# Performance work log

Hardware: AMD Instinct MI355X
Metric: run time of the kernel (lower is better)

Reference implementation:

```python
import jax, jax.numpy as jnp
import numpy as np

V, E, C, H = 50000, 300, 128, 128
B, SC, SE = 128, 512, 64


def gru_scan(x, lengths, gate_w, gate_b, cand_w, cand_b):
    """TF GRUCell dynamic_rnn: x [B,S,E] -> outputs [B,S,C], zeroed past lengths."""
    Bn, S, _ = x.shape
    Cn = cand_w.shape[1]

    def step(h, inp):
        xt, t = inp  # xt [B,E]
        ru = jax.nn.sigmoid(jnp.concatenate([xt, h], axis=-1) @ gate_w + gate_b)
        r, u = jnp.split(ru, 2, axis=-1)
        c = jnp.tanh(jnp.concatenate([xt, r * h], axis=-1) @ cand_w + cand_b)
        hn = u * h + (1.0 - u) * c
        active = (t < lengths)[:, None]
        hn = jnp.where(active, hn, h)
        out = jnp.where(active, hn, 0.0)
        return hn, out

    h0 = jnp.zeros((Bn, Cn), dtype=x.dtype)
    _, outs = jax.lax.scan(step, h0, (jnp.swapaxes(x, 0, 1), jnp.arange(S)))
    return jnp.swapaxes(outs, 0, 1)


def reverse_seq(x, lengths):
    """tf.reverse_sequence along time for [B,S,D]."""
    S = x.shape[1]
    t = jnp.arange(S)[None, :]
    L = lengths[:, None]
    idx = jnp.where(t < L, L - 1 - t, t)
    return jnp.take_along_axis(x, idx[:, :, None], axis=1)


def attend(states, att_v, att_w, att_b):
    # states [B,S,C]
    scores = jnp.einsum('bsd,d->bs', jnp.tanh(jnp.einsum('bsc,cd->bsd', states, att_w) + att_b), att_v)
    w = jax.nn.softmax(scores, axis=1)
    return jnp.einsum('bsc,bs->bc', states, w)


def extract_features(seq, lengths, embeddings,
                     fw_gate_w, fw_gate_b, fw_cand_w, fw_cand_b,
                     bw_gate_w, bw_gate_b, bw_cand_w, bw_cand_b,
                     att_v, att_w, att_b):
    emb = embeddings[seq]  # [B,S,E]
    fw_states = gru_scan(emb, lengths, fw_gate_w, fw_gate_b, fw_cand_w, fw_cand_b)
    emb_rev = reverse_seq(emb, lengths)
    bw_out = gru_scan(emb_rev, lengths, bw_gate_w, bw_gate_b, bw_cand_w, bw_cand_b)
    bw_states = reverse_seq(bw_out, lengths)
    fw_c = attend(fw_states, att_v, att_w, att_b)
    bw_c = attend(bw_states, att_v, att_w, att_b)
    return jnp.concatenate([fw_c, bw_c], axis=1)


def setup_inputs() -> dict:
    key = jax.random.key(0)
    ks = jax.random.split(key, 20)
    s = 0.05
    context = jax.random.randint(ks[0], (B, SC), 0, V, dtype=jnp.int32)
    end = jax.random.randint(ks[1], (B, SE), 0, V, dtype=jnp.int32)
    context_length = jnp.clip(jax.random.randint(ks[2], (B,), 1, SC + 1), 1, SC).astype(jnp.int32)
    end_length = jnp.clip(jax.random.randint(ks[3], (B,), 1, SE + 1), 1, SE).astype(jnp.int32)
    return {
        'context': context, 'end': end,
        'context_length': context_length, 'end_length': end_length,
        'embeddings': jax.random.normal(ks[4], (V, E), jnp.float32) * s,
        'fw_gate_w': jax.random.normal(ks[5], (E + C, 2 * C), jnp.float32) * s,
        'fw_gate_b': jnp.ones((2 * C,), jnp.float32),
        'fw_cand_w': jax.random.normal(ks[6], (E + C, C), jnp.float32) * s,
        'fw_cand_b': jnp.zeros((C,), jnp.float32),
        'bw_gate_w': jax.random.normal(ks[7], (E + C, 2 * C), jnp.float32) * s,
        'bw_gate_b': jnp.ones((2 * C,), jnp.float32),
        'bw_cand_w': jax.random.normal(ks[8], (E + C, C), jnp.float32) * s,
        'bw_cand_b': jnp.zeros((C,), jnp.float32),
        'att_v': jax.random.normal(ks[9], (C,), jnp.float32) * s,
        'att_w': jax.random.normal(ks[10], (C, C), jnp.float32) * s,
        'att_b': jnp.zeros((C,), jnp.float32),
        'hid_w': jax.random.normal(ks[11], (4 * C, H), jnp.float32) * s,
        'hid_b': jnp.zeros((H,), jnp.float32),
        'out_w': jax.random.normal(ks[12], (H, 1), jnp.float32) * s,
        'out_b': jnp.zeros((1,), jnp.float32),
    }


def reference(context, end, context_length, end_length, embeddings,
              fw_gate_w, fw_gate_b, fw_cand_w, fw_cand_b,
              bw_gate_w, bw_gate_b, bw_cand_w, bw_cand_b,
              att_v, att_w, att_b, hid_w, hid_b, out_w, out_b):
    ctx_f = extract_features(context, context_length, embeddings,
                             fw_gate_w, fw_gate_b, fw_cand_w, fw_cand_b,
                             bw_gate_w, bw_gate_b, bw_cand_w, bw_cand_b,
                             att_v, att_w, att_b)
    end_f = extract_features(end, end_length, embeddings,
                             fw_gate_w, fw_gate_b, fw_cand_w, fw_cand_b,
                             bw_gate_w, bw_gate_b, bw_cand_w, bw_cand_b,
                             att_v, att_w, att_b)
    feats = jnp.concatenate([ctx_f, end_f], axis=1)  # [B, 4C]
    hidden = jax.nn.relu(feats @ hid_w + hid_b)
    logit = (hidden @ out_w + out_b)[:, 0]  # [B]
    return logit
```

## Files before the change

### kernel.cpp

```cpp
#include <hip/hip_runtime.h>
#include <cstdint>
#include <cmath>

static constexpr int V_  = 50000;
static constexpr int E_  = 300;
static constexpr int C_  = 128;
static constexpr int B_  = 128;
static constexpr int SC_ = 512;
static constexpr int SE_ = 64;
static constexpr int NCOL = 768;
static constexpr int KP  = 320;

static constexpr size_t OFF_PROJ  = 0;
static constexpr size_t SZ_PROJ   = (size_t)V_ * NCOL;
static constexpr size_t OFF_WXP   = OFF_PROJ + SZ_PROJ;
static constexpr size_t SZ_WXP    = (size_t)304 * NCOL;
static constexpr size_t OFF_UALL  = OFF_WXP + SZ_WXP;
static constexpr size_t SZ_UALL   = (size_t)C_ * NCOL;
static constexpr size_t OFF_BIAS  = OFF_UALL + SZ_UALL;
static constexpr size_t SZ_BIAS   = NCOL;
static constexpr size_t OFF_ST    = OFF_BIAS + SZ_BIAS;
static constexpr size_t SZ_ST_CTX = (size_t)B_ * SC_ * C_;
static constexpr size_t SZ_ST_END = (size_t)B_ * SE_ * C_;
static constexpr size_t SZ_ST     = 2*SZ_ST_CTX + 2*SZ_ST_END;
static constexpr size_t OFF_FEATS = OFF_ST + SZ_ST;
static constexpr size_t SZ_FEATS  = (size_t)B_ * 512;
static constexpr size_t OFF_BT    = OFF_FEATS + SZ_FEATS;
static constexpr size_t SZ_BT     = (size_t)NCOL * KP / 2 * 2;
static constexpr size_t OFF_AWT   = OFF_BT + SZ_BT;

typedef __attribute__((ext_vector_type(8))) short bf16x8;
typedef __attribute__((ext_vector_type(4))) float f32x4;

static __device__ __forceinline__ unsigned short f2bf_rne(float f) {
  unsigned u = __float_as_uint(f);
  unsigned r = u + 0x7fffu + ((u >> 16) & 1u);
  return (unsigned short)(r >> 16);
}

static __device__ __forceinline__ void gload_lds16(const short* g, short* l) {
  __builtin_amdgcn_global_load_lds(
      (const __attribute__((address_space(1))) void*)g,
      (__attribute__((address_space(3))) void*)l, 16, 0, 0);
}

static __device__ __forceinline__ float fast_sigmoid(float x) {
  return __builtin_amdgcn_rcpf(1.f + __expf(-x));
}
static __device__ __forceinline__ float fast_tanh(float x) {
  return fmaf(-2.f, __builtin_amdgcn_rcpf(__expf(2.f * x) + 1.f), 1.f);
}

__global__ void pack_kernel(const float* __restrict__ fw_gw, const float* __restrict__ fw_gb,
                            const float* __restrict__ fw_cw, const float* __restrict__ fw_cb,
                            const float* __restrict__ bw_gw, const float* __restrict__ bw_gb,
                            const float* __restrict__ bw_cw, const float* __restrict__ bw_cb,
                            float* __restrict__ ws) {
  int i = blockIdx.x * 256 + threadIdx.x;
  float* Wxp  = ws + OFF_WXP;
  float* Uall = ws + OFF_UALL;
  float* bias = ws + OFF_BIAS;
  if (i < 304 * NCOL) {
    int k = i / NCOL, c = i % NCOL;
    float v = 0.f;
    if (k < 300) {
      if (c < 256)      v = fw_gw[k*256 + c];
      else if (c < 384) v = fw_cw[k*128 + (c-256)];
      else if (c < 640) v = bw_gw[k*256 + (c-384)];
      else              v = bw_cw[k*128 + (c-640)];
    }
    Wxp[i] = v;
    return;
  }
  int j = i - 304 * NCOL;
  if (j >= 0 && j < 128 * NCOL) {
    int k = j / NCOL, c = j % NCOL;
    int kk = 300 + k;
    float v;
    if (c < 256)      v = fw_gw[kk*256 + c];
    else if (c < 384) v = fw_cw[kk*128 + (c-256)];
    else if (c < 640) v = bw_gw[kk*256 + (c-384)];
    else              v = bw_cw[kk*128 + (c-640)];
    Uall[j] = v;
    return;
  }
  int m = j - 128 * NCOL;
  if (m >= 0 && m < NCOL) {
    float v;
    if (m < 256)      v = fw_gb[m];
    else if (m < 384) v = fw_cb[m-256];
    else if (m < 640) v = bw_gb[m-384];
    else              v = bw_cb[m-640];
    bias[m] = v;
  }
}

__global__ void pack_bt(const float* __restrict__ Wxp, short* __restrict__ Bthi,
                        short* __restrict__ Btlo, const float* __restrict__ att_w,
                        short* __restrict__ awt_hi, short* __restrict__ awt_lo) {
  int i = blockIdx.x * 256 + threadIdx.x;
  if (i < NCOL * KP) {
    int k = i % KP, n = i / KP;
    float v = (k < 304) ? Wxp[(size_t)k * NCOL + n] : 0.f;
    unsigned short h = f2bf_rne(v);
    float hf = __uint_as_float((unsigned)h << 16);
    unsigned short lo = f2bf_rne(v - hf);
    Bthi[i] = (short)h;
    Btlo[i] = (short)lo;
    return;
  }
  int j = i - NCOL * KP;
  if (j < 128 * 128) {
    int d = j >> 7, c = j & 127;
    float v = att_w[(size_t)c * 128 + d];
    unsigned short h = f2bf_rne(v);
    float hf = __uint_as_float((unsigned)h << 16);
    unsigned short lo = f2bf_rne(v - hf);
    awt_hi[j] = (short)h;
    awt_lo[j] = (short)lo;
  }
}

__global__ void pack_emb(const float* __restrict__ emb, short* __restrict__ Ahi,
                         short* __restrict__ Alo) {
  size_t i = (size_t)blockIdx.x * 256 + threadIdx.x;
  if (i >= (size_t)V_ * KP) return;
  int k = (int)(i % KP);
  size_t row = i / KP;
  float v = (k < E_) ? emb[row * E_ + k] : 0.f;
  unsigned short h = f2bf_rne(v);
  float hf = __uint_as_float((unsigned)h << 16);
  unsigned short lo = f2bf_rne(v - hf);
  Ahi[i] = (short)h;
  Alo[i] = (short)lo;
}

__global__ __launch_bounds__(256) void gemm_mfma(
    const short* __restrict__ Ahi, const short* __restrict__ Alo,
    const short* __restrict__ Bthi, const short* __restrict__ Btlo,
    float* __restrict__ proj) {
  __shared__ short lds[16384];
  int tid = threadIdx.x, wid = tid >> 6, lane = tid & 63;
  int n0 = blockIdx.x * 128, m0 = blockIdx.y * 128;
  f32x4 acc[4][4] = {};

  int lr = lane >> 2, lc = lane & 3;
  int q0 = wid * 2, q1 = q0 + 1;
  int r0 = q0 * 16 + lr, r1 = q1 * 16 + lr;
  int am0 = m0 + r0; if (am0 > V_ - 1) am0 = V_ - 1;
  int am1 = m0 + r1; if (am1 > V_ - 1) am1 = V_ - 1;
  size_t gaOff0 = (size_t)am0 * KP + lc * 8;
  size_t gaOff1 = (size_t)am1 * KP + lc * 8;
  size_t gbOff0 = (size_t)(n0 + r0) * KP + lc * 8;
  size_t gbOff1 = (size_t)(n0 + r1) * KP + lc * 8;

  int quad = lane >> 4;
  int arow = (wid >> 1) * 64 + (lane & 15);
  int brow = (wid & 1) * 64 + (lane & 15);

  for (int k0 = 0; k0 < KP; k0 += 32) {
    gload_lds16(Ahi  + gaOff0 + k0, lds +         q0 * 512);
    gload_lds16(Ahi  + gaOff1 + k0, lds +         q1 * 512);
    gload_lds16(Alo  + gaOff0 + k0, lds +  4096 + q0 * 512);
    gload_lds16(Alo  + gaOff1 + k0, lds +  4096 + q1 * 512);
    gload_lds16(Bthi + gbOff0 + k0, lds +  8192 + q0 * 512);
    gload_lds16(Bthi + gbOff1 + k0, lds +  8192 + q1 * 512);
    gload_lds16(Btlo + gbOff0 + k0, lds + 12288 + q0 * 512);
    gload_lds16(Btlo + gbOff1 + k0, lds + 12288 + q1 * 512);
    __syncthreads();

    bf16x8 ah[4], al[4], bh[4], bl[4];
#pragma unroll
    for (int i = 0; i < 4; ++i) {
      ah[i] = *(bf16x8*)&lds[        (arow + i*16) * 32 + quad * 8];
      al[i] = *(bf16x8*)&lds[ 4096 + (arow + i*16) * 32 + quad * 8];
      bh[i] = *(bf16x8*)&lds[ 8192 + (brow + i*16) * 32 + quad * 8];
      bl[i] = *(bf16x8*)&lds[12288 + (brow + i*16) * 32 + quad * 8];
    }
#pragma unroll
    for (int i = 0; i < 4; ++i)
#pragma unroll
      for (int j = 0; j < 4; ++j) {
        acc[i][j] = __builtin_amdgcn_mfma_f32_16x16x32_bf16(ah[i], bh[j], acc[i][j], 0, 0, 0);
        acc[i][j] = __builtin_amdgcn_mfma_f32_16x16x32_bf16(ah[i], bl[j], acc[i][j], 0, 0, 0);
        acc[i][j] = __builtin_amdgcn_mfma_f32_16x16x32_bf16(al[i], bh[j], acc[i][j], 0, 0, 0);
      }
    __syncthreads();
  }

  int colb = n0 + (wid & 1) * 64 + (lane & 15);
  int rowb = m0 + (wid >> 1) * 64 + quad * 4;
#pragma unroll
  for (int i = 0; i < 4; ++i) {
    int rb = rowb + i * 16;
#pragma unroll
    for (int j = 0; j < 4; ++j) {
      int cc = colb + j * 16;
#pragma unroll
      for (int r = 0; r < 4; ++r) {
        int rr = rb + r;
        if (rr < V_) proj[(size_t)rr * NCOL + cc] = acc[i][j][r];
      }
    }
  }
}

__global__ __attribute__((amdgpu_flat_work_group_size(256, 256),
                          amdgpu_waves_per_eu(2, 2)))
void recur_kernel(
    const int* __restrict__ ctx, const int* __restrict__ endseq,
    const int* __restrict__ ctx_len, const int* __restrict__ end_len,
    const float* __restrict__ proj, const float* __restrict__ Uall,
    const float* __restrict__ bias, float* __restrict__ states) {
  __shared__ __align__(16) float h_s[128];
  __shared__ __align__(16) float rh_s[128];
  __shared__ __align__(16) float u_s[128];
  __shared__ __align__(16) float pg[8][260];
  __shared__ __align__(16) float pc[8][132];

  int bid = blockIdx.x;
  int tid = threadIdx.x;
  const int* seq; int S, L, b, dir; float* stbase;
  if (bid < 256) {
    b = bid >> 1; dir = bid & 1;
    seq = ctx + b * SC_; S = SC_; L = ctx_len[b];
    stbase = states + (dir ? SZ_ST_CTX : 0) + (size_t)b * SC_ * C_;
  } else {
    int q = bid - 256; b = q >> 1; dir = q & 1;
    seq = endseq + b * SE_; S = SE_; L = end_len[b];
    stbase = states + 2*SZ_ST_CTX + (dir ? SZ_ST_END : 0) + (size_t)b * SE_ * C_;
  }
  int dirOff = dir ? 384 : 0;
  int kg = tid >> 5, jg = tid & 31;

  float wg[16][8];
  float wc[16][4];
#pragma unroll
  for (int kk = 0; kk < 16; ++kk) {
    const float* up = Uall + (size_t)(kg*16 + kk) * NCOL + dirOff;
    float4 w0 = *(const float4*)(up + jg*8);
    float4 w1 = *(const float4*)(up + jg*8 + 4);
    wg[kk][0]=w0.x; wg[kk][1]=w0.y; wg[kk][2]=w0.z; wg[kk][3]=w0.w;
    wg[kk][4]=w1.x; wg[kk][5]=w1.y; wg[kk][6]=w1.z; wg[kk][7]=w1.w;
    float4 wv = *(const float4*)(up + 256 + jg*4);
    wc[kk][0]=wv.x; wc[kk][1]=wv.y; wc[kk][2]=wv.z; wc[kk][3]=wv.w;
  }
  float bias_g = bias[dirOff + tid];
  float bias_c = (tid < 128) ? bias[dirOff + 256 + tid] : 0.f;

  if (tid < 128) h_s[tid] = 0.f;
  __syncthreads();

  int pos0 = dir ? (L - 1) : 0;
  int tok0 = seq[pos0];
  const float* xr0 = proj + (size_t)tok0 * NCOL + dirOff;
  float xg = xr0[tid];
  float xc = (tid < 128) ? xr0[256 + tid] : 0.f;

  for (int t = 0; t < L; ++t) {
    float xg_n = 0.f, xc_n = 0.f;
    if (t + 1 < L) {
      int pos_n = dir ? (L - 2 - t) : (t + 1);
      int tok_n = seq[pos_n];
      const float* xr = proj + (size_t)tok_n * NCOL + dirOff;
      xg_n = xr[tid];
      xc_n = (tid < 128) ? xr[256 + tid] : 0.f;
    }

    float a[8] = {0.f,0.f,0.f,0.f,0.f,0.f,0.f,0.f};
    const float4* h4 = (const float4*)h_s;
#pragma unroll
    for (int q = 0; q < 4; ++q) {
      float4 hv = h4[kg*4 + q];
      float he[4] = {hv.x, hv.y, hv.z, hv.w};
#pragma unroll
      for (int e = 0; e < 4; ++e)
#pragma unroll
        for (int jj = 0; jj < 8; ++jj)
          a[jj] += he[e] * wg[q*4 + e][jj];
    }
    *(float4*)(&pg[kg][jg*8])     = make_float4(a[0], a[1], a[2], a[3]);
    *(float4*)(&pg[kg][jg*8 + 4]) = make_float4(a[4], a[5], a[6], a[7]);
    __syncthreads();

    float g = xg + bias_g;
#pragma unroll
    for (int k2 = 0; k2 < 8; ++k2) g += pg[k2][tid];
    g = fast_sigmoid(g);

    float h_old = 0.f;
    if (tid < 128) { h_old = h_s[tid]; rh_s[tid] = g * h_old; }
    else           { u_s[tid - 128] = g; }
    __syncthreads();

    float ac[4] = {0.f, 0.f, 0.f, 0.f};
    const float4* rh4 = (const float4*)rh_s;
#pragma unroll
    for (int q = 0; q < 4; ++q) {
      float4 rv = rh4[kg*4 + q];
      float re[4] = {rv.x, rv.y, rv.z, rv.w};
#pragma unroll
      for (int e = 0; e < 4; ++e)
#pragma unroll
        for (int jj = 0; jj < 4; ++jj)
          ac[jj] += re[e] * wc[q*4 + e][jj];
    }
    *(float4*)(&pc[kg][jg*4]) = make_float4(ac[0], ac[1], ac[2], ac[3]);
    __syncthreads();

    if (tid < 128) {
      float cs = xc + bias_c;
#pragma unroll
      for (int k2 = 0; k2 < 8; ++k2) cs += pc[k2][tid];
      float c = fast_tanh(cs);
      float u = u_s[tid];
      float hn = u * h_old + (1.f - u) * c;
      h_s[tid] = hn;
      int pos = dir ? (L - 1 - t) : t;
      stbase[(size_t)pos * C_ + tid] = hn;
    }
    __syncthreads();
    xg = xg_n; xc = xc_n;
  }

  for (int i = L * C_ + tid; i < S * C_; i += 256) stbase[i] = 0.f;
}

__global__ __launch_bounds__(256, 2) void attn_kernel(
    const float* __restrict__ states, const short* __restrict__ awt_hi,
    const short* __restrict__ awt_lo, const float* __restrict__ att_v,
    const float* __restrict__ att_b, float* __restrict__ feats) {
  __shared__ __align__(16) float st_s[16][132];
  __shared__ __align__(16) short ah_s[16][132];
  __shared__ __align__(16) short al_s[16][132];
  __shared__ float spart[4][16];
  __shared__ float score_s[16];
  __shared__ float cm[128], cl[128], ca[128];

  int bid = blockIdx.x, tid = threadIdx.x;
  int b, dir, S, featOff; const float* stb;
  if (bid < 256) {
    b = bid >> 1; dir = bid & 1; S = SC_;
    stb = states + (dir ? SZ_ST_CTX : 0) + (size_t)b * SC_ * C_;
    featOff = dir * 128;
  } else {
    int q = bid - 256; b = q >> 1; dir = q & 1; S = SE_;
    stb = states + 2*SZ_ST_CTX + (dir ? SZ_ST_END : 0) + (size_t)b * SE_ * C_;
    featOff = 256 + dir * 128;
  }

  int w = tid >> 6, lane = tid & 63;
  int quad = lane >> 4, l15 = lane & 15;

  int d0 = 32 * w + l15, d1 = d0 + 16;
  bf16x8 bh0[4], bh1[4], bl0[4], bl1[4];
#pragma unroll
  for (int kt = 0; kt < 4; ++kt) {
    bh0[kt] = *(const bf16x8*)&awt_hi[d0*128 + kt*32 + quad*8];
    bh1[kt] = *(const bf16x8*)&awt_hi[d1*128 + kt*32 + quad*8];
    bl0[kt] = *(const bf16x8*)&awt_lo[d0*128 + kt*32 + quad*8];
    bl1[kt] = *(const bf16x8*)&awt_lo[d1*128 + kt*32 + quad*8];
  }
  float vv0 = att_v[d0], vv1 = att_v[d1];
  float bb0 = att_b[d0], bb1 = att_b[d1];

  int c = tid & 127, half = tid >> 7;
  float m = -1e30f, lsum = 0.f, acc = 0.f;

  int lrow = tid >> 4, lcol = (tid & 15) * 8;
  float4 p0, p1;
  {
    const float* src = stb + (size_t)lrow * C_ + lcol;
    p0 = *(const float4*)(src);
    p1 = *(const float4*)(src + 4);
  }

  int nchunks = S >> 4;
  for (int ch = 0; ch < nchunks; ++ch) {
    __syncthreads();
    float f[8] = {p0.x, p0.y, p0.z, p0.w, p1.x, p1.y, p1.z, p1.w};
    short hi8[8], lo8[8];
#pragma unroll
    for (int j = 0; j < 8; ++j) {
      unsigned short h = f2bf_rne(f[j]);
      float hf = __uint_as_float((unsigned)h << 16);
      hi8[j] = (short)h;
      lo8[j] = (short)f2bf_rne(f[j] - hf);
    }
    *(float4*)(&st_s[lrow][lcol])     = p0;
    *(float4*)(&st_s[lrow][lcol + 4]) = p1;
    *(bf16x8*)(&ah_s[lrow][lcol]) = *(bf16x8*)hi8;
    *(bf16x8*)(&al_s[lrow][lcol]) = *(bf16x8*)lo8;
    if (ch + 1 < nchunks) {
      const float* src = stb + (size_t)((ch + 1) * 16 + lrow) * C_ + lcol;
      p0 = *(const float4*)(src);
      p1 = *(const float4*)(src + 4);
    }
    __syncthreads();

    f32x4 ac0 = {0.f, 0.f, 0.f, 0.f}, ac1 = {0.f, 0.f, 0.f, 0.f};
#pragma unroll
    for (int kt = 0; kt < 4; ++kt) {
      bf16x8 a_hi = *(bf16x8*)&ah_s[l15][kt*32 + quad*8];
      bf16x8 a_lo = *(bf16x8*)&al_s[l15][kt*32 + quad*8];
      ac0 = __builtin_amdgcn_mfma_f32_16x16x32_bf16(a_hi, bh0[kt], ac0, 0, 0, 0);
      ac0 = __builtin_amdgcn_mfma_f32_16x16x32_bf16(a_hi, bl0[kt], ac0, 0, 0, 0);
      ac0 = __builtin_amdgcn_mfma_f32_16x16x32_bf16(a_lo, bh0[kt], ac0, 0, 0, 0);
      ac1 = __builtin_amdgcn_mfma_f32_16x16x32_bf16(a_hi, bh1[kt], ac1, 0, 0, 0);
      ac1 = __builtin_amdgcn_mfma_f32_16x16x32_bf16(a_hi, bl1[kt], ac1, 0, 0, 0);
      ac1 = __builtin_amdgcn_mfma_f32_16x16x32_bf16(a_lo, bh1[kt], ac1, 0, 0, 0);
    }

    float part[4];
#pragma unroll
    for (int r = 0; r < 4; ++r)
      part[r] = fast_tanh(ac0[r] + bb0) * vv0 + fast_tanh(ac1[r] + bb1) * vv1;
#pragma unroll
    for (int mask = 1; mask <= 8; mask <<= 1)
#pragma unroll
      for (int r = 0; r < 4; ++r)
        part[r] += __shfl_xor(part[r], mask, 64);
    if (l15 == 0) {
#pragma unroll
      for (int r = 0; r < 4; ++r) spart[w][quad*4 + r] = part[r];
    }
    __syncthreads();
    if (tid < 16)
      score_s[tid] = spart[0][tid] + spart[1][tid] + spart[2][tid] + spart[3][tid];
    __syncthreads();

    float srow[8]; float smax = m;
#pragma unroll
    for (int r = 0; r < 8; ++r) { srow[r] = score_s[half*8 + r]; smax = fmaxf(smax, srow[r]); }
    float scale = __expf(m - smax);
    acc *= scale; lsum *= scale; m = smax;
#pragma unroll
    for (int r = 0; r < 8; ++r) {
      float wgt = __expf(srow[r] - m);
      lsum += wgt;
      acc += wgt * st_s[half*8 + r][c];
    }
  }

  __syncthreads();
  if (half == 1) { cm[c] = m; cl[c] = lsum; ca[c] = acc; }
  __syncthreads();
  if (half == 0) {
    float m1 = cm[c], l1 = cl[c], a1 = ca[c];
    float M = fmaxf(m, m1);
    float w0 = __expf(m - M), w1 = __expf(m1 - M);
    feats[b * 512 + featOff + c] = (acc * w0 + a1 * w1) / (lsum * w0 + l1 * w1);
  }
}

__global__ __launch_bounds__(128) void head_kernel(
    const float* __restrict__ feats, const float* __restrict__ hid_w,
    const float* __restrict__ hid_b, const float* __restrict__ out_w,
    const float* __restrict__ out_b, float* __restrict__ out) {
  __shared__ __align__(16) float f_s[512];
  __shared__ float part[2];
  int b = blockIdx.x, tid = threadIdx.x;
  for (int i = tid; i < 512; i += 128) f_s[i] = feats[b * 512 + i];
  __syncthreads();
  float h = hid_b[tid];
  for (int k = 0; k < 512; ++k) h += f_s[k] * hid_w[k * 128 + tid];
  h = fmaxf(h, 0.f);
  float p = h * out_w[tid];
#pragma unroll
  for (int off = 32; off > 0; off >>= 1) p += __shfl_xor(p, off, 64);
  if ((tid & 63) == 0) part[tid >> 6] = p;
  __syncthreads();
  if (tid == 0) out[b] = part[0] + part[1] + out_b[0];
}

extern "C" void kernel_launch(void* const* d_in, const int* in_sizes, int n_in,
                              void* d_out, int out_size, void* d_ws, size_t ws_size,
                              hipStream_t stream) {
  const int*   ctx     = (const int*)d_in[0];
  const int*   endseq  = (const int*)d_in[1];
  const int*   ctx_len = (const int*)d_in[2];
  const int*   end_len = (const int*)d_in[3];
  const float* emb     = (const float*)d_in[4];
  const float* fw_gw   = (const float*)d_in[5];
  const float* fw_gb   = (const float*)d_in[6];
  const float* fw_cw   = (const float*)d_in[7];
  const float* fw_cb   = (const float*)d_in[8];
  const float* bw_gw   = (const float*)d_in[9];
  const float* bw_gb   = (const float*)d_in[10];
  const float* bw_cw   = (const float*)d_in[11];
  const float* bw_cb   = (const float*)d_in[12];
  const float* att_v   = (const float*)d_in[13];
  const float* att_w   = (const float*)d_in[14];
  const float* att_b   = (const float*)d_in[15];
  const float* hid_w   = (const float*)d_in[16];
  const float* hid_b   = (const float*)d_in[17];
  const float* out_w   = (const float*)d_in[18];
  const float* out_b   = (const float*)d_in[19];
  float* ws  = (float*)d_ws;
  float* out = (float*)d_out;

  short* Ahi    = (short*)(ws + OFF_ST);
  short* Alo    = Ahi + (size_t)V_ * KP;
  short* Bthi   = (short*)(ws + OFF_BT);
  short* Btlo   = Bthi + (size_t)NCOL * KP;
  short* awt_hi = (short*)(ws + OFF_AWT);
  short* awt_lo = awt_hi + 128 * 128;

  pack_kernel<<<1299, 256, 0, stream>>>(fw_gw, fw_gb, fw_cw, fw_cb,
                                        bw_gw, bw_gb, bw_cw, bw_cb, ws);
  pack_bt<<<(NCOL * KP + 128 * 128 + 255) / 256, 256, 0, stream>>>(
      ws + OFF_WXP, Bthi, Btlo, att_w, awt_hi, awt_lo);
  pack_emb<<<(int)(((size_t)V_ * KP + 255) / 256), 256, 0, stream>>>(emb, Ahi, Alo);

  dim3 ggrid(6, 391);
  gemm_mfma<<<ggrid, 256, 0, stream>>>(Ahi, Alo, Bthi, Btlo, ws + OFF_PROJ);

  recur_kernel<<<512, 256, 0, stream>>>(ctx, endseq, ctx_len, end_len,
                                        ws + OFF_PROJ, ws + OFF_UALL,
                                        ws + OFF_BIAS, ws + OFF_ST);

  attn_kernel<<<512, 256, 0, stream>>>(ws + OFF_ST, awt_hi, awt_lo,
                                       att_v, att_b, ws + OFF_FEATS);

  head_kernel<<<128, 128, 0, stream>>>(ws + OFF_FEATS, hid_w, hid_b,
                                       out_w, out_b, out);
}
```

Before: 768.4 us.

## Process two batch sequences per recurrence block to share register-held weights

The GRU recurrence kernel now runs two batch rows (same direction) in each workgroup. The recurrent weights held in registers are reused for both sequences' matvecs, and each barrier covers both sequences. This halves the grid to 256 blocks and gives each wave more independent work to hide latency. In exchange the loop runs to the longer of the two lengths, so the shorter sequence does wasted steps, and waves-per-EU drops to one.

```diff
diff --git a/kernel.cpp b/kernel.cpp
--- a/kernel.cpp
+++ b/kernel.cpp
@@ -206,29 +206,37 @@
 }
 
 __global__ __attribute__((amdgpu_flat_work_group_size(256, 256),
-                          amdgpu_waves_per_eu(2, 2)))
-void recur_kernel(
+                          amdgpu_waves_per_eu(1, 1)))
+void recur_pair_kernel(
     const int* __restrict__ ctx, const int* __restrict__ endseq,
     const int* __restrict__ ctx_len, const int* __restrict__ end_len,
     const float* __restrict__ proj, const float* __restrict__ Uall,
     const float* __restrict__ bias, float* __restrict__ states) {
-  __shared__ __align__(16) float h_s[128];
-  __shared__ __align__(16) float rh_s[128];
-  __shared__ __align__(16) float u_s[128];
-  __shared__ __align__(16) float pg[8][260];
-  __shared__ __align__(16) float pc[8][132];
+  __shared__ __align__(16) float h_sA[128],  h_sB[128];
+  __shared__ __align__(16) float rh_sA[128], rh_sB[128];
+  __shared__ __align__(16) float u_sA[128],  u_sB[128];
+  __shared__ __align__(16) float pgA[8][260], pgB[8][260];
+  __shared__ __align__(16) float pcA[8][132], pcB[8][132];
 
   int bid = blockIdx.x;
   int tid = threadIdx.x;
-  const int* seq; int S, L, b, dir; float* stbase;
-  if (bid < 256) {
-    b = bid >> 1; dir = bid & 1;
-    seq = ctx + b * SC_; S = SC_; L = ctx_len[b];
-    stbase = states + (dir ? SZ_ST_CTX : 0) + (size_t)b * SC_ * C_;
+  const int *seqA, *seqB; int S, LA, LB, dir; float *stA, *stB;
+  if (bid < 128) {
+    dir = bid & 1; int p = bid >> 1;
+    int b0 = p * 2, b1 = b0 + 1;
+    seqA = ctx + b0 * SC_; seqB = ctx + b1 * SC_;
+    S = SC_; LA = ctx_len[b0]; LB = ctx_len[b1];
+    float* base = states + (dir ? SZ_ST_CTX : 0);
+    stA = base + (size_t)b0 * SC_ * C_;
+    stB = base + (size_t)b1 * SC_ * C_;
   } else {
-    int q = bid - 256; b = q >> 1; dir = q & 1;
-    seq = endseq + b * SE_; S = SE_; L = end_len[b];
-    stbase = states + 2*SZ_ST_CTX + (dir ? SZ_ST_END : 0) + (size_t)b * SE_ * C_;
+    int q = bid - 128; dir = q & 1; int p = q >> 1;
+    int b0 = p * 2, b1 = b0 + 1;
+    seqA = endseq + b0 * SE_; seqB = endseq + b1 * SE_;
+    S = SE_; LA = end_len[b0]; LB = end_len[b1];
+    float* base = states + 2*SZ_ST_CTX + (dir ? SZ_ST_END : 0);
+    stA = base + (size_t)b0 * SE_ * C_;
+    stB = base + (size_t)b1 * SE_ * C_;
   }
   int dirOff = dir ? 384 : 0;
   int kg = tid >> 5, jg = tid & 31;
@@ -248,82 +256,131 @@
   float bias_g = bias[dirOff + tid];
   float bias_c = (tid < 128) ? bias[dirOff + 256 + tid] : 0.f;
 
-  if (tid < 128) h_s[tid] = 0.f;
+  if (tid < 128) { h_sA[tid] = 0.f; h_sB[tid] = 0.f; }
   __syncthreads();
 
-  int pos0 = dir ? (L - 1) : 0;
-  int tok0 = seq[pos0];
-  const float* xr0 = proj + (size_t)tok0 * NCOL + dirOff;
-  float xg = xr0[tid];
-  float xc = (tid < 128) ? xr0[256 + tid] : 0.f;
-
-  for (int t = 0; t < L; ++t) {
-    float xg_n = 0.f, xc_n = 0.f;
-    if (t + 1 < L) {
-      int pos_n = dir ? (L - 2 - t) : (t + 1);
-      int tok_n = seq[pos_n];
+  int Lm = (LA > LB) ? LA : LB;
+
+  int posA0 = dir ? (LA - 1) : 0;
+  int tokA0 = seqA[posA0];
+  const float* xrA0 = proj + (size_t)tokA0 * NCOL + dirOff;
+  float xgA = xrA0[tid];
+  float xcA = (tid < 128) ? xrA0[256 + tid] : 0.f;
+  int posB0 = dir ? (LB - 1) : 0;
+  int tokB0 = seqB[posB0];
+  const float* xrB0 = proj + (size_t)tokB0 * NCOL + dirOff;
+  float xgB = xrB0[tid];
+  float xcB = (tid < 128) ? xrB0[256 + tid] : 0.f;
+
+  for (int t = 0; t < Lm; ++t) {
+    float xgA_n = 0.f, xcA_n = 0.f, xgB_n = 0.f, xcB_n = 0.f;
+    if (t + 1 < LA) {
+      int pos_n = dir ? (LA - 2 - t) : (t + 1);
+      int tok_n = seqA[pos_n];
       const float* xr = proj + (size_t)tok_n * NCOL + dirOff;
-      xg_n = xr[tid];
-      xc_n = (tid < 128) ? xr[256 + tid] : 0.f;
-    }
-
-    float a[8] = {0.f,0.f,0.f,0.f,0.f,0.f,0.f,0.f};
-    const float4* h4 = (const float4*)h_s;
+      xgA_n = xr[tid];
+      xcA_n = (tid < 128) ? xr[256 + tid] : 0.f;
+    }
+    if (t + 1 < LB) {
+      int pos_n = dir ? (LB - 2 - t) : (t + 1);
+      int tok_n = seqB[pos_n];
+      const float* xr = proj + (size_t)tok_n * NCOL + dirOff;
+      xgB_n = xr[tid];
+      xcB_n = (tid < 128) ? xr[256 + tid] : 0.f;
+    }
+
+    float aA[8] = {0.f,0.f,0.f,0.f,0.f,0.f,0.f,0.f};
+    float aB[8] = {0.f,0.f,0.f,0.f,0.f,0.f,0.f,0.f};
+    const float4* h4A = (const float4*)h_sA;
+    const float4* h4B = (const float4*)h_sB;
 #pragma unroll
     for (int q = 0; q < 4; ++q) {
-      float4 hv = h4[kg*4 + q];
-      float he[4] = {hv.x, hv.y, hv.z, hv.w};
+      float4 hvA = h4A[kg*4 + q];
+      float4 hvB = h4B[kg*4 + q];
+      float heA[4] = {hvA.x, hvA.y, hvA.z, hvA.w};
+      float heB[4] = {hvB.x, hvB.y, hvB.z, hvB.w};
 #pragma unroll
       for (int e = 0; e < 4; ++e)
 #pragma unroll
-        for (int jj = 0; jj < 8; ++jj)
-          a[jj] += he[e] * wg[q*4 + e][jj];
-    }
-    *(float4*)(&pg[kg][jg*8])     = make_float4(a[0], a[1], a[2], a[3]);
-    *(float4*)(&pg[kg][jg*8 + 4]) = make_float4(a[4], a[5], a[6], a[7]);
-    __syncthreads();
-
-    float g = xg + bias_g;
-#pragma unroll
-    for (int k2 = 0; k2 < 8; ++k2) g += pg[k2][tid];
-    g = fast_sigmoid(g);
-
-    float h_old = 0.f;
-    if (tid < 128) { h_old = h_s[tid]; rh_s[tid] = g * h_old; }
-    else           { u_s[tid - 128] = g; }
-    __syncthreads();
-
-    float ac[4] = {0.f, 0.f, 0.f, 0.f};
-    const float4* rh4 = (const float4*)rh_s;
+        for (int jj = 0; jj < 8; ++jj) {
+          aA[jj] += heA[e] * wg[q*4 + e][jj];
+          aB[jj] += heB[e] * wg[q*4 + e][jj];
+        }
+    }
+    *(float4*)(&pgA[kg][jg*8])     = make_float4(aA[0], aA[1], aA[2], aA[3]);
+    *(float4*)(&pgA[kg][jg*8 + 4]) = make_float4(aA[4], aA[5], aA[6], aA[7]);
+    *(float4*)(&pgB[kg][jg*8])     = make_float4(aB[0], aB[1], aB[2], aB[3]);
+    *(float4*)(&pgB[kg][jg*8 + 4]) = make_float4(aB[4], aB[5], aB[6], aB[7]);
+    __syncthreads();
+
+    float gA = xgA + bias_g;
+    float gB = xgB + bias_g;
+#pragma unroll
+    for (int k2 = 0; k2 < 8; ++k2) { gA += pgA[k2][tid]; gB += pgB[k2][tid]; }
+    gA = fast_sigmoid(gA);
+    gB = fast_sigmoid(gB);
+
+    float h_oldA = 0.f, h_oldB = 0.f;
+    if (tid < 128) {
+      h_oldA = h_sA[tid]; rh_sA[tid] = gA * h_oldA;
+      h_oldB = h_sB[tid]; rh_sB[tid] = gB * h_oldB;
+    } else {
+      u_sA[tid - 128] = gA;
+      u_sB[tid - 128] = gB;
+    }
+    __syncthreads();
+
+    float acA[4] = {0.f, 0.f, 0.f, 0.f};
+    float acB[4] = {0.f, 0.f, 0.f, 0.f};
+    const float4* rh4A = (const float4*)rh_sA;
+    const float4* rh4B = (const float4*)rh_sB;
 #pragma unroll
     for (int q = 0; q < 4; ++q) {
-      float4 rv = rh4[kg*4 + q];
-      float re[4] = {rv.x, rv.y, rv.z, rv.w};
+      float4 rvA = rh4A[kg*4 + q];
+      float4 rvB = rh4B[kg*4 + q];
+      float reA[4] = {rvA.x, rvA.y, rvA.z, rvA.w};
+      float reB[4] = {rvB.x, rvB.y, rvB.z, rvB.w};
 #pragma unroll
       for (int e = 0; e < 4; ++e)
 #pragma unroll
-        for (int jj = 0; jj < 4; ++jj)
-          ac[jj] += re[e] * wc[q*4 + e][jj];
-    }
-    *(float4*)(&pc[kg][jg*4]) = make_float4(ac[0], ac[1], ac[2], ac[3]);
+        for (int jj = 0; jj < 4; ++jj) {
+          acA[jj] += reA[e] * wc[q*4 + e][jj];
+          acB[jj] += reB[e] * wc[q*4 + e][jj];
+        }
+    }
+    *(float4*)(&pcA[kg][jg*4]) = make_float4(acA[0], acA[1], acA[2], acA[3]);
+    *(float4*)(&pcB[kg][jg*4]) = make_float4(acB[0], acB[1], acB[2], acB[3]);
     __syncthreads();
 
     if (tid < 128) {
-      float cs = xc + bias_c;
-#pragma unroll
-      for (int k2 = 0; k2 < 8; ++k2) cs += pc[k2][tid];
-      float c = fast_tanh(cs);
-      float u = u_s[tid];
-      float hn = u * h_old + (1.f - u) * c;
-      h_s[tid] = hn;
-      int pos = dir ? (L - 1 - t) : t;
-      stbase[(size_t)pos * C_ + tid] = hn;
-    }
-    __syncthreads();
-    xg = xg_n; xc = xc_n;
-  }
-
-  for (int i = L * C_ + tid; i < S * C_; i += 256) stbase[i] = 0.f;
+      float csA = xcA + bias_c;
+      float csB = xcB + bias_c;
+#pragma unroll
+      for (int k2 = 0; k2 < 8; ++k2) { csA += pcA[k2][tid]; csB += pcB[k2][tid]; }
+      float cA = fast_tanh(csA);
+      float cB = fast_tanh(csB);
+      float uA = u_sA[tid];
+      float uB = u_sB[tid];
+      float hnA = uA * h_oldA + (1.f - uA) * cA;
+      float hnB = uB * h_oldB + (1.f - uB) * cB;
+      h_sA[tid] = hnA;
+      h_sB[tid] = hnB;
+      if (t < LA) {
+        int pos = dir ? (LA - 1 - t) : t;
+        stA[(size_t)pos * C_ + tid] = hnA;
+      }
+      if (t < LB) {
+        int pos = dir ? (LB - 1 - t) : t;
+        stB[(size_t)pos * C_ + tid] = hnB;
+      }
+    }
+    __syncthreads();
+    xgA = xgA_n; xcA = xcA_n;
+    xgB = xgB_n; xcB = xcB_n;
+  }
+
+  for (int i = LA * C_ + tid; i < S * C_; i += 256) stA[i] = 0.f;
+  for (int i = LB * C_ + tid; i < S * C_; i += 256) stB[i] = 0.f;
 }
 
 __global__ __launch_bounds__(256, 2) void attn_kernel(
@@ -515,9 +572,9 @@
   dim3 ggrid(6, 391);
   gemm_mfma<<<ggrid, 256, 0, stream>>>(Ahi, Alo, Bthi, Btlo, ws + OFF_PROJ);
 
-  recur_kernel<<<512, 256, 0, stream>>>(ctx, endseq, ctx_len, end_len,
-                                        ws + OFF_PROJ, ws + OFF_UALL,
-                                        ws + OFF_BIAS, ws + OFF_ST);
+  recur_pair_kernel<<<256, 256, 0, stream>>>(ctx, endseq, ctx_len, end_len,
+                                             ws + OFF_PROJ, ws + OFF_UALL,
+                                             ws + OFF_BIAS, ws + OFF_ST);
 
   attn_kernel<<<512, 256, 0, stream>>>(ws + OFF_ST, awt_hi, awt_lo,
                                        att_v, att_b, ws + OFF_FEATS);
```

New measurement: 1.068 ms. 1.39x slower.

## Repartition GRU recurrence matvec to pairs of lanes with shuffle reduction

Applied to the files above, without the earlier changes.

Replaces the 8-way k-split matvec with LDS partial-sum buffers by a per-thread layout where each thread owns one gate column (and one candidate column shared by a lane pair) over half the hidden dimension. A new pack kernel rearranges the recurrent weights so each thread loads its slice contiguously into registers. Partial sums are combined with a single lane shuffle instead of LDS writes, which removes two of the four barriers per timestep on the serial critical path. It adds a small extra pack launch and redundant candidate work on both lanes of each pair.

```diff
diff --git a/kernel.cpp b/kernel.cpp
--- a/kernel.cpp
+++ b/kernel.cpp
@@ -28,6 +28,8 @@
 static constexpr size_t OFF_BT    = OFF_FEATS + SZ_FEATS;
 static constexpr size_t SZ_BT     = (size_t)NCOL * KP / 2 * 2;
 static constexpr size_t OFF_AWT   = OFF_BT + SZ_BT;
+static constexpr size_t OFF_WPK   = OFF_AWT + 16384;
+static constexpr size_t SZ_WPK    = 98304;
 
 typedef __attribute__((ext_vector_type(8))) short bf16x8;
 typedef __attribute__((ext_vector_type(4))) float f32x4;
@@ -95,6 +97,31 @@
   }
 }
 
+__global__ void pack_w2(const float* __restrict__ fw_gw, const float* __restrict__ bw_gw,
+                        const float* __restrict__ fw_cw, const float* __restrict__ bw_cw,
+                        float* __restrict__ wpack) {
+  int i = blockIdx.x * 256 + threadIdx.x;
+  if (i < 65536) {
+    int d = i >> 15, r = i & 32767;
+    int t = r >> 7, kk = r & 127;
+    int kl = kk >> 1, cp = kk & 1;
+    int k = (t & 1) * 64 + kl;
+    int col = (t & ~1) | cp;
+    const float* gw = d ? bw_gw : fw_gw;
+    wpack[i] = gw[(300 + k) * 256 + col];
+    return;
+  }
+  int j = i - 65536;
+  if (j < 32768) {
+    int d = j >> 14, r = j & 16383;
+    int t = r >> 6, kl = r & 63;
+    int k = (t & 1) * 64 + kl;
+    int cc = t >> 1;
+    const float* cw = d ? bw_cw : fw_cw;
+    wpack[65536 + j] = cw[(300 + k) * 128 + cc];
+  }
+}
+
 __global__ void pack_bt(const float* __restrict__ Wxp, short* __restrict__ Bthi,
                         short* __restrict__ Btlo, const float* __restrict__ att_w,
                         short* __restrict__ awt_hi, short* __restrict__ awt_lo) {
@@ -207,19 +234,16 @@
 
 __global__ __attribute__((amdgpu_flat_work_group_size(256, 256),
                           amdgpu_waves_per_eu(2, 2)))
-void recur_kernel(
+void recur2_kernel(
     const int* __restrict__ ctx, const int* __restrict__ endseq,
     const int* __restrict__ ctx_len, const int* __restrict__ end_len,
-    const float* __restrict__ proj, const float* __restrict__ Uall,
+    const float* __restrict__ proj, const float* __restrict__ wpack,
     const float* __restrict__ bias, float* __restrict__ states) {
   __shared__ __align__(16) float h_s[128];
   __shared__ __align__(16) float rh_s[128];
-  __shared__ __align__(16) float u_s[128];
-  __shared__ __align__(16) float pg[8][260];
-  __shared__ __align__(16) float pc[8][132];
-
-  int bid = blockIdx.x;
-  int tid = threadIdx.x;
+  __shared__ float u_s[128];
+
+  int bid = blockIdx.x, tid = threadIdx.x;
   const int* seq; int S, L, b, dir; float* stbase;
   if (bid < 256) {
     b = bid >> 1; dir = bid & 1;
@@ -231,93 +255,77 @@
     stbase = states + 2*SZ_ST_CTX + (dir ? SZ_ST_END : 0) + (size_t)b * SE_ * C_;
   }
   int dirOff = dir ? 384 : 0;
-  int kg = tid >> 5, jg = tid & 31;
-
-  float wg[16][8];
-  float wc[16][4];
-#pragma unroll
-  for (int kk = 0; kk < 16; ++kk) {
-    const float* up = Uall + (size_t)(kg*16 + kk) * NCOL + dirOff;
-    float4 w0 = *(const float4*)(up + jg*8);
-    float4 w1 = *(const float4*)(up + jg*8 + 4);
-    wg[kk][0]=w0.x; wg[kk][1]=w0.y; wg[kk][2]=w0.z; wg[kk][3]=w0.w;
-    wg[kk][4]=w1.x; wg[kk][5]=w1.y; wg[kk][6]=w1.z; wg[kk][7]=w1.w;
-    float4 wv = *(const float4*)(up + 256 + jg*4);
-    wc[kk][0]=wv.x; wc[kk][1]=wv.y; wc[kk][2]=wv.z; wc[kk][3]=wv.w;
+  int c = tid >> 1, kh = tid & 1;
+  int hbase = kh * 16;
+
+  float4 wgt[32], wct[16];
+  {
+    const float4* wgp = (const float4*)(wpack + ((size_t)dir * 256 + tid) * 128);
+    const float4* wcp = (const float4*)(wpack + 65536 + ((size_t)dir * 256 + tid) * 64);
+#pragma unroll
+    for (int i = 0; i < 32; ++i) wgt[i] = wgp[i];
+#pragma unroll
+    for (int i = 0; i < 16; ++i) wct[i] = wcp[i];
   }
   float bias_g = bias[dirOff + tid];
-  float bias_c = (tid < 128) ? bias[dirOff + 256 + tid] : 0.f;
+  float bias_c = bias[dirOff + 256 + c];
 
   if (tid < 128) h_s[tid] = 0.f;
   __syncthreads();
 
   int pos0 = dir ? (L - 1) : 0;
-  int tok0 = seq[pos0];
-  const float* xr0 = proj + (size_t)tok0 * NCOL + dirOff;
+  const float* xr0 = proj + (size_t)seq[pos0] * NCOL + dirOff;
   float xg = xr0[tid];
-  float xc = (tid < 128) ? xr0[256 + tid] : 0.f;
+  float xc = xr0[256 + c];
 
   for (int t = 0; t < L; ++t) {
     float xg_n = 0.f, xc_n = 0.f;
     if (t + 1 < L) {
       int pos_n = dir ? (L - 2 - t) : (t + 1);
-      int tok_n = seq[pos_n];
-      const float* xr = proj + (size_t)tok_n * NCOL + dirOff;
+      const float* xr = proj + (size_t)seq[pos_n] * NCOL + dirOff;
       xg_n = xr[tid];
-      xc_n = (tid < 128) ? xr[256 + tid] : 0.f;
-    }
-
-    float a[8] = {0.f,0.f,0.f,0.f,0.f,0.f,0.f,0.f};
+      xc_n = xr[256 + c];
+    }
+
+    float a0 = 0.f, a1 = 0.f, a2 = 0.f, a3 = 0.f;
     const float4* h4 = (const float4*)h_s;
 #pragma unroll
-    for (int q = 0; q < 4; ++q) {
-      float4 hv = h4[kg*4 + q];
-      float he[4] = {hv.x, hv.y, hv.z, hv.w};
-#pragma unroll
-      for (int e = 0; e < 4; ++e)
-#pragma unroll
-        for (int jj = 0; jj < 8; ++jj)
-          a[jj] += he[e] * wg[q*4 + e][jj];
-    }
-    *(float4*)(&pg[kg][jg*8])     = make_float4(a[0], a[1], a[2], a[3]);
-    *(float4*)(&pg[kg][jg*8 + 4]) = make_float4(a[4], a[5], a[6], a[7]);
-    __syncthreads();
-
-    float g = xg + bias_g;
-#pragma unroll
-    for (int k2 = 0; k2 < 8; ++k2) g += pg[k2][tid];
-    g = fast_sigmoid(g);
-
-    float h_old = 0.f;
-    if (tid < 128) { h_old = h_s[tid]; rh_s[tid] = g * h_old; }
-    else           { u_s[tid - 128] = g; }
-    __syncthreads();
-
-    float ac[4] = {0.f, 0.f, 0.f, 0.f};
+    for (int i = 0; i < 16; ++i) {
+      float4 hv = h4[hbase + i];
+      float4 w0 = wgt[2*i], w1 = wgt[2*i + 1];
+      a0 = fmaf(hv.x, w0.x, a0); a1 = fmaf(hv.x, w0.y, a1);
+      a2 = fmaf(hv.y, w0.z, a2); a3 = fmaf(hv.y, w0.w, a3);
+      a0 = fmaf(hv.z, w1.x, a0); a1 = fmaf(hv.z, w1.y, a1);
+      a2 = fmaf(hv.w, w1.z, a2); a3 = fmaf(hv.w, w1.w, a3);
+    }
+    float pa0 = a0 + a2, pa1 = a1 + a3;
+    float g0 = pa0 + __shfl_xor(pa0, 1, 64);
+    float g1 = pa1 + __shfl_xor(pa1, 1, 64);
+    float g = fast_sigmoid(((tid & 1) ? g1 : g0) + xg + bias_g);
+
+    if (tid < 128) rh_s[tid] = g * h_s[tid];
+    else           u_s[tid - 128] = g;
+    __syncthreads();
+
+    float c0 = 0.f, c1 = 0.f, c2 = 0.f, c3 = 0.f;
     const float4* rh4 = (const float4*)rh_s;
 #pragma unroll
-    for (int q = 0; q < 4; ++q) {
-      float4 rv = rh4[kg*4 + q];
-      float re[4] = {rv.x, rv.y, rv.z, rv.w};
-#pragma unroll
-      for (int e = 0; e < 4; ++e)
-#pragma unroll
-        for (int jj = 0; jj < 4; ++jj)
-          ac[jj] += re[e] * wc[q*4 + e][jj];
-    }
-    *(float4*)(&pc[kg][jg*4]) = make_float4(ac[0], ac[1], ac[2], ac[3]);
-    __syncthreads();
-
-    if (tid < 128) {
-      float cs = xc + bias_c;
-#pragma unroll
-      for (int k2 = 0; k2 < 8; ++k2) cs += pc[k2][tid];
-      float c = fast_tanh(cs);
-      float u = u_s[tid];
-      float hn = u * h_old + (1.f - u) * c;
-      h_s[tid] = hn;
+    for (int i = 0; i < 16; ++i) {
+      float4 rv = rh4[hbase + i];
+      float4 w = wct[i];
+      c0 = fmaf(rv.x, w.x, c0); c1 = fmaf(rv.y, w.y, c1);
+      c2 = fmaf(rv.z, w.z, c2); c3 = fmaf(rv.w, w.w, c3);
+    }
+    float ac = (c0 + c1) + (c2 + c3);
+    ac += __shfl_xor(ac, 1, 64);
+    float cd = fast_tanh(ac + xc + bias_c);
+    float u  = u_s[c];
+    float ho = h_s[c];
+    float hn = u * ho + (1.f - u) * cd;
+    if (!kh) {
+      h_s[c] = hn;
       int pos = dir ? (L - 1 - t) : t;
-      stbase[(size_t)pos * C_ + tid] = hn;
+      stbase[(size_t)pos * C_ + c] = hn;
     }
     __syncthreads();
     xg = xg_n; xc = xc_n;
@@ -508,6 +516,7 @@
 
   pack_kernel<<<1299, 256, 0, stream>>>(fw_gw, fw_gb, fw_cw, fw_cb,
                                         bw_gw, bw_gb, bw_cw, bw_cb, ws);
+  pack_w2<<<384, 256, 0, stream>>>(fw_gw, bw_gw, fw_cw, bw_cw, ws + OFF_WPK);
   pack_bt<<<(NCOL * KP + 128 * 128 + 255) / 256, 256, 0, stream>>>(
       ws + OFF_WXP, Bthi, Btlo, att_w, awt_hi, awt_lo);
   pack_emb<<<(int)(((size_t)V_ * KP + 255) / 256), 256, 0, stream>>>(emb, Ahi, Alo);
@@ -515,9 +524,9 @@
   dim3 ggrid(6, 391);
   gemm_mfma<<<ggrid, 256, 0, stream>>>(Ahi, Alo, Bthi, Btlo, ws + OFF_PROJ);
 
-  recur_kernel<<<512, 256, 0, stream>>>(ctx, endseq, ctx_len, end_len,
-                                        ws + OFF_PROJ, ws + OFF_UALL,
-                                        ws + OFF_BIAS, ws + OFF_ST);
+  recur2_kernel<<<512, 256, 0, stream>>>(ctx, endseq, ctx_len, end_len,
+                                         ws + OFF_PROJ, ws + OFF_WPK,
+                                         ws + OFF_BIAS, ws + OFF_ST);
 
   attn_kernel<<<512, 256, 0, stream>>>(ws + OFF_ST, awt_hi, awt_lo,
                                        att_v, att_b, ws + OFF_FEATS);
```

Measured after the change: 851.1 us. +10.8%, slower.

## Fuse GRU recurrence with attention and remap GEMM blocks per XCD

Applied to the files above, without the earlier changes.

Merges the recurrence and attention kernels into one launch: each block runs its GRU scan, then reuses the same aliased shared memory to compute attention over the states it just wrote. This removes a kernel launch and lets attention start per block without waiting for all recurrences, and the states may still be cache-resident. Separately, the GEMM grid is flattened and block IDs are remapped so consecutive tiles land on the same XCD, for better L2 locality. The fused kernel keeps the recurrence's waves_per_eu constraint, which may limit the attention phase's register budget.

```diff
diff --git a/kernel.cpp b/kernel.cpp
--- a/kernel.cpp
+++ b/kernel.cpp
@@ -141,7 +141,13 @@
     float* __restrict__ proj) {
   __shared__ short lds[16384];
   int tid = threadIdx.x, wid = tid >> 6, lane = tid & 63;
-  int n0 = blockIdx.x * 128, m0 = blockIdx.y * 128;
+
+  int bid = blockIdx.x;
+  int xcd = bid & 7, idx = bid >> 3;
+  int wgid = (xcd < 2 ? xcd * 294 : 588 + (xcd - 2) * 293) + idx;
+  int m0 = (wgid / 6) * 128;
+  int n0 = (wgid % 6) * 128;
+
   f32x4 acc[4][4] = {};
 
   int lr = lane >> 2, lc = lane & 3;
@@ -207,148 +213,142 @@
 
 __global__ __attribute__((amdgpu_flat_work_group_size(256, 256),
                           amdgpu_waves_per_eu(2, 2)))
-void recur_kernel(
+void recur_attn_kernel(
     const int* __restrict__ ctx, const int* __restrict__ endseq,
     const int* __restrict__ ctx_len, const int* __restrict__ end_len,
     const float* __restrict__ proj, const float* __restrict__ Uall,
-    const float* __restrict__ bias, float* __restrict__ states) {
-  __shared__ __align__(16) float h_s[128];
-  __shared__ __align__(16) float rh_s[128];
-  __shared__ __align__(16) float u_s[128];
-  __shared__ __align__(16) float pg[8][260];
-  __shared__ __align__(16) float pc[8][132];
+    const float* __restrict__ bias, float* __restrict__ states,
+    const short* __restrict__ awt_hi, const short* __restrict__ awt_lo,
+    const float* __restrict__ att_v, const float* __restrict__ att_b,
+    float* __restrict__ feats) {
+  __shared__ __align__(16) char smraw[18752];
+  float* h_s  = (float*)smraw;
+  float* rh_s = h_s + 128;
+  float* u_s  = rh_s + 128;
+  float (*pg)[260] = (float(*)[260])(u_s + 128);
+  float (*pc)[132] = (float(*)[132])(pg + 8);
+  float (*st_s)[132] = (float(*)[132])smraw;
+  short (*ah_s)[132] = (short(*)[132])(smraw + 8448);
+  short (*al_s)[132] = (short(*)[132])(smraw + 12672);
+  float (*spart)[16] = (float(*)[16])(smraw + 16896);
+  float* score_s = (float*)(smraw + 17152);
+  float* cm = (float*)(smraw + 17216);
+  float* cl = cm + 128;
+  float* ca = cl + 128;
 
   int bid = blockIdx.x;
   int tid = threadIdx.x;
-  const int* seq; int S, L, b, dir; float* stbase;
+  const int* seq; int S, L, b, dir, featOff; float* stbase;
   if (bid < 256) {
     b = bid >> 1; dir = bid & 1;
     seq = ctx + b * SC_; S = SC_; L = ctx_len[b];
     stbase = states + (dir ? SZ_ST_CTX : 0) + (size_t)b * SC_ * C_;
+    featOff = dir * 128;
   } else {
     int q = bid - 256; b = q >> 1; dir = q & 1;
     seq = endseq + b * SE_; S = SE_; L = end_len[b];
     stbase = states + 2*SZ_ST_CTX + (dir ? SZ_ST_END : 0) + (size_t)b * SE_ * C_;
+    featOff = 256 + dir * 128;
   }
   int dirOff = dir ? 384 : 0;
   int kg = tid >> 5, jg = tid & 31;
 
-  float wg[16][8];
-  float wc[16][4];
-#pragma unroll
-  for (int kk = 0; kk < 16; ++kk) {
-    const float* up = Uall + (size_t)(kg*16 + kk) * NCOL + dirOff;
-    float4 w0 = *(const float4*)(up + jg*8);
-    float4 w1 = *(const float4*)(up + jg*8 + 4);
-    wg[kk][0]=w0.x; wg[kk][1]=w0.y; wg[kk][2]=w0.z; wg[kk][3]=w0.w;
-    wg[kk][4]=w1.x; wg[kk][5]=w1.y; wg[kk][6]=w1.z; wg[kk][7]=w1.w;
-    float4 wv = *(const float4*)(up + 256 + jg*4);
-    wc[kk][0]=wv.x; wc[kk][1]=wv.y; wc[kk][2]=wv.z; wc[kk][3]=wv.w;
-  }
-  float bias_g = bias[dirOff + tid];
-  float bias_c = (tid < 128) ? bias[dirOff + 256 + tid] : 0.f;
-
-  if (tid < 128) h_s[tid] = 0.f;
+  {
+    float wg[16][8];
+    float wc[16][4];
+#pragma unroll
+    for (int kk = 0; kk < 16; ++kk) {
+      const float* up = Uall + (size_t)(kg*16 + kk) * NCOL + dirOff;
+      float4 w0 = *(const float4*)(up + jg*8);
+      float4 w1 = *(const float4*)(up + jg*8 + 4);
+      wg[kk][0]=w0.x; wg[kk][1]=w0.y; wg[kk][2]=w0.z; wg[kk][3]=w0.w;
+      wg[kk][4]=w1.x; wg[kk][5]=w1.y; wg[kk][6]=w1.z; wg[kk][7]=w1.w;
+      float4 wv = *(const float4*)(up + 256 + jg*4);
+      wc[kk][0]=wv.x; wc[kk][1]=wv.y; wc[kk][2]=wv.z; wc[kk][3]=wv.w;
+    }
+    float bias_g = bias[dirOff + tid];
+    float bias_c = (tid < 128) ? bias[dirOff + 256 + tid] : 0.f;
+
+    if (tid < 128) h_s[tid] = 0.f;
+    __syncthreads();
+
+    int pos0 = dir ? (L - 1) : 0;
+    int tok0 = seq[pos0];
+    const float* xr0 = proj + (size_t)tok0 * NCOL + dirOff;
+    float xg = xr0[tid];
+    float xc = (tid < 128) ? xr0[256 + tid] : 0.f;
+
+    for (int t = 0; t < L; ++t) {
+      float xg_n = 0.f, xc_n = 0.f;
+      if (t + 1 < L) {
+        int pos_n = dir ? (L - 2 - t) : (t + 1);
+        int tok_n = seq[pos_n];
+        const float* xr = proj + (size_t)tok_n * NCOL + dirOff;
+        xg_n = xr[tid];
+        xc_n = (tid < 128) ? xr[256 + tid] : 0.f;
+      }
+
+      float a[8] = {0.f,0.f,0.f,0.f,0.f,0.f,0.f,0.f};
+      const float4* h4 = (const float4*)h_s;
+#pragma unroll
+      for (int q = 0; q < 4; ++q) {
+        float4 hv = h4[kg*4 + q];
+        float he[4] = {hv.x, hv.y, hv.z, hv.w};
+#pragma unroll
+        for (int e = 0; e < 4; ++e)
+#pragma unroll
+          for (int jj = 0; jj < 8; ++jj)
+            a[jj] += he[e] * wg[q*4 + e][jj];
+      }
+      *(float4*)(&pg[kg][jg*8])     = make_float4(a[0], a[1], a[2], a[3]);
+      *(float4*)(&pg[kg][jg*8 + 4]) = make_float4(a[4], a[5], a[6], a[7]);
+      __syncthreads();
+
+      float g = xg + bias_g;
+#pragma unroll
+      for (int k2 = 0; k2 < 8; ++k2) g += pg[k2][tid];
+      g = fast_sigmoid(g);
+
+      float h_old = 0.f;
+      if (tid < 128) { h_old = h_s[tid]; rh_s[tid] = g * h_old; }
+      else           { u_s[tid - 128] = g; }
+      __syncthreads();
+
+      float ac[4] = {0.f, 0.f, 0.f, 0.f};
+      const float4* rh4 = (const float4*)rh_s;
+#pragma unroll
+      for (int q = 0; q < 4; ++q) {
+        float4 rv = rh4[kg*4 + q];
+        float re[4] = {rv.x, rv.y, rv.z, rv.w};
+#pragma unroll
+        for (int e = 0; e < 4; ++e)
+#pragma unroll
+          for (int jj = 0; jj < 4; ++jj)
+            ac[jj] += re[e] * wc[q*4 + e][jj];
+      }
+      *(float4*)(&pc[kg][jg*4]) = make_float4(ac[0], ac[1], ac[2], ac[3]);
+      __syncthreads();
+
+      if (tid < 128) {
+        float cs = xc + bias_c;
+#pragma unroll
+        for (int k2 = 0; k2 < 8; ++k2) cs += pc[k2][tid];
+        float c = fast_tanh(cs);
+        float u = u_s[tid];
+        float hn = u * h_old + (1.f - u) * c;
+        h_s[tid] = hn;
+        int pos = dir ? (L - 1 - t) : t;
+        stbase[(size_t)pos * C_ + tid] = hn;
+      }
+      __syncthreads();
+      xg = xg_n; xc = xc_n;
+    }
+
+    for (int i = L * C_ + tid; i < S * C_; i += 256) stbase[i] = 0.f;
+  }
   __syncthreads();
 
-  int pos0 = dir ? (L - 1) : 0;
-  int tok0 = seq[pos0];
-  const float* xr0 = proj + (size_t)tok0 * NCOL + dirOff;
-  float xg = xr0[tid];
-  float xc = (tid < 128) ? xr0[256 + tid] : 0.f;
-
-  for (int t = 0; t < L; ++t) {
-    float xg_n = 0.f, xc_n = 0.f;
-    if (t + 1 < L) {
-      int pos_n = dir ? (L - 2 - t) : (t + 1);
-      int tok_n = seq[pos_n];
-      const float* xr = proj + (size_t)tok_n * NCOL + dirOff;
-      xg_n = xr[tid];
-      xc_n = (tid < 128) ? xr[256 + tid] : 0.f;
-    }
-
-    float a[8] = {0.f,0.f,0.f,0.f,0.f,0.f,0.f,0.f};
-    const float4* h4 = (const float4*)h_s;
-#pragma unroll
-    for (int q = 0; q < 4; ++q) {
-      float4 hv = h4[kg*4 + q];
-      float he[4] = {hv.x, hv.y, hv.z, hv.w};
-#pragma unroll
-      for (int e = 0; e < 4; ++e)
-#pragma unroll
-        for (int jj = 0; jj < 8; ++jj)
-          a[jj] += he[e] * wg[q*4 + e][jj];
-    }
-    *(float4*)(&pg[kg][jg*8])     = make_float4(a[0], a[1], a[2], a[3]);
-    *(float4*)(&pg[kg][jg*8 + 4]) = make_float4(a[4], a[5], a[6], a[7]);
-    __syncthreads();
-
-    float g = xg + bias_g;
-#pragma unroll
-    for (int k2 = 0; k2 < 8; ++k2) g += pg[k2][tid];
-    g = fast_sigmoid(g);
-
-    float h_old = 0.f;
-    if (tid < 128) { h_old = h_s[tid]; rh_s[tid] = g * h_old; }
-    else           { u_s[tid - 128] = g; }
-    __syncthreads();
-
-    float ac[4] = {0.f, 0.f, 0.f, 0.f};
-    const float4* rh4 = (const float4*)rh_s;
-#pragma unroll
-    for (int q = 0; q < 4; ++q) {
-      float4 rv = rh4[kg*4 + q];
-      float re[4] = {rv.x, rv.y, rv.z, rv.w};
-#pragma unroll
-      for (int e = 0; e < 4; ++e)
-#pragma unroll
-        for (int jj = 0; jj < 4; ++jj)
-          ac[jj] += re[e] * wc[q*4 + e][jj];
-    }
-    *(float4*)(&pc[kg][jg*4]) = make_float4(ac[0], ac[1], ac[2], ac[3]);
-    __syncthreads();
-
-    if (tid < 128) {
-      float cs = xc + bias_c;
-#pragma unroll
-      for (int k2 = 0; k2 < 8; ++k2) cs += pc[k2][tid];
-      float c = fast_tanh(cs);
-      float u = u_s[tid];
-      float hn = u * h_old + (1.f - u) * c;
-      h_s[tid] = hn;
-      int pos = dir ? (L - 1 - t) : t;
-      stbase[(size_t)pos * C_ + tid] = hn;
-    }
-    __syncthreads();
-    xg = xg_n; xc = xc_n;
-  }
-
-  for (int i = L * C_ + tid; i < S * C_; i += 256) stbase[i] = 0.f;
-}
-
-__global__ __launch_bounds__(256, 2) void attn_kernel(
-    const float* __restrict__ states, const short* __restrict__ awt_hi,
-    const short* __restrict__ awt_lo, const float* __restrict__ att_v,
-    const float* __restrict__ att_b, float* __restrict__ feats) {
-  __shared__ __align__(16) float st_s[16][132];
-  __shared__ __align__(16) short ah_s[16][132];
-  __shared__ __align__(16) short al_s[16][132];
-  __shared__ float spart[4][16];
-  __shared__ float score_s[16];
-  __shared__ float cm[128], cl[128], ca[128];
-
-  int bid = blockIdx.x, tid = threadIdx.x;
-  int b, dir, S, featOff; const float* stb;
-  if (bid < 256) {
-    b = bid >> 1; dir = bid & 1; S = SC_;
-    stb = states + (dir ? SZ_ST_CTX : 0) + (size_t)b * SC_ * C_;
-    featOff = dir * 128;
-  } else {
-    int q = bid - 256; b = q >> 1; dir = q & 1; S = SE_;
-    stb = states + 2*SZ_ST_CTX + (dir ? SZ_ST_END : 0) + (size_t)b * SE_ * C_;
-    featOff = 256 + dir * 128;
-  }
-
+  const float* stb = stbase;
   int w = tid >> 6, lane = tid & 63;
   int quad = lane >> 4, l15 = lane & 15;
 
@@ -512,15 +512,13 @@
       ws + OFF_WXP, Bthi, Btlo, att_w, awt_hi, awt_lo);
   pack_emb<<<(int)(((size_t)V_ * KP + 255) / 256), 256, 0, stream>>>(emb, Ahi, Alo);
 
-  dim3 ggrid(6, 391);
-  gemm_mfma<<<ggrid, 256, 0, stream>>>(Ahi, Alo, Bthi, Btlo, ws + OFF_PROJ);
-
-  recur_kernel<<<512, 256, 0, stream>>>(ctx, endseq, ctx_len, end_len,
-                                        ws + OFF_PROJ, ws + OFF_UALL,
-                                        ws + OFF_BIAS, ws + OFF_ST);
-
-  attn_kernel<<<512, 256, 0, stream>>>(ws + OFF_ST, awt_hi, awt_lo,
-                                       att_v, att_b, ws + OFF_FEATS);
+  gemm_mfma<<<2346, 256, 0, stream>>>(Ahi, Alo, Bthi, Btlo, ws + OFF_PROJ);
+
+  recur_attn_kernel<<<512, 256, 0, stream>>>(ctx, endseq, ctx_len, end_len,
+                                             ws + OFF_PROJ, ws + OFF_UALL,
+                                             ws + OFF_BIAS, ws + OFF_ST,
+                                             awt_hi, awt_lo, att_v, att_b,
+                                             ws + OFF_FEATS);
 
   head_kernel<<<128, 128, 0, stream>>>(ws + OFF_FEATS, hid_w, hid_b,
                                        out_w, out_b, out);
```

Measured after the change: 768.4 us. Within noise of the previous version (+0.0%).
